# Kernel tuning notes

Measured on AMD Instinct MI355X. Metric: run time of the kernel, lower is better.

## Reference

```python
import jax, jax.numpy as jnp
import numpy as np

N_NODES = 50000


def setup_inputs() -> dict:
    key = jax.random.key(0)
    k1, k2, k3, k4 = jax.random.split(key, 4)
    x = jax.random.normal(k1, (N_NODES, 128), dtype=jnp.float32)
    edge_index = jax.random.randint(k2, (2, 1600000), 0, N_NODES, dtype=jnp.int64)
    W1 = jax.random.normal(k3, (128, 256), dtype=jnp.float32) * (1.0 / np.sqrt(128))
    b1 = jnp.zeros((256,), dtype=jnp.float32)
    W2 = jax.random.normal(k4, (256, 1), dtype=jnp.float32) * (1.0 / np.sqrt(256))
    b2 = jnp.zeros((1,), dtype=jnp.float32)
    return {"x": x, "edge_index": edge_index, "W1": W1, "b1": b1, "W2": W2, "b2": b2}


def _gcn_conv(x, src, dst, norm, W, b, n_nodes):
    # PyG GCNConv: h = X W; out_i = sum_j norm_ij * h_j (+ self loop) + b
    h = x @ W                               # [N, F_out]
    msg = h[src] * norm[:, None]            # [E', F_out] gather + scale
    out = jax.ops.segment_sum(msg, dst, num_segments=n_nodes)  # scatter-add
    return out + b


def reference(x, edge_index, W1, b1, W2, b2):
    n = x.shape[0]
    loop = jnp.arange(n, dtype=edge_index.dtype)
    src = jnp.concatenate([edge_index[0], loop])   # add self loops
    dst = jnp.concatenate([edge_index[1], loop])
    # symmetric degree normalization on A + I
    deg = jax.ops.segment_sum(jnp.ones_like(dst, dtype=x.dtype), dst, num_segments=n)
    dis = jnp.where(deg > 0, jax.lax.rsqrt(deg), 0.0)
    norm = dis[src] * dis[dst]                     # [E']
    h = jax.nn.relu(_gcn_conv(x, src, dst, norm, W1, b1, n))
    return _gcn_conv(h, src, dst, norm, W2, b2, n)
```

## Files before the change

kernel.cpp:

```cpp
#include <hip/hip_runtime.h>


#define EPB_LOG 12
#define EPB (1 << EPB_LOG)
#define BW_LOG 7
#define BW (1 << BW_LOG)
#define MAXBUCK 512
#define SCAN_TILE 2048
#define AMSTRIDE 136

typedef __attribute__((ext_vector_type(8))) short bf16x8;
typedef __attribute__((ext_vector_type(4))) float f32x4;

__device__ inline unsigned short f2bf(float f) {
    unsigned int b = __float_as_uint(f);
    unsigned int r = b + 0x7FFFu + ((b >> 16) & 1u);
    return (unsigned short)(r >> 16);
}
__device__ inline float bf_lo(unsigned int u) { return __uint_as_float(u << 16); }
__device__ inline float bf_hi(unsigned int u) { return __uint_as_float(u & 0xFFFF0000u); }

__device__ inline int detect_stride(const int* edges, int t, int* sh) {
    if (t < 64) {
        int v = edges[2 * t + 1];
        unsigned long long bb = __ballot(v != 0);
        if (t == 0) *sh = bb ? 1 : 2;
    }
    __syncthreads();
    return *sh;
}


__global__ __launch_bounds__(256) void k_count(
        const int* __restrict__ edges, const float* __restrict__ W1,
        unsigned short* __restrict__ w1t, int* __restrict__ btot_raw,
        long long E, int nbuck, int nsb) {
    int b = blockIdx.x, t = threadIdx.x;
    if (b >= nsb) {
        int row = (b - nsb) * 2 + (t >> 7);
        int k = t & 127;
        w1t[row * 128 + k] = f2bf(W1[k * 256 + row]);
        return;
    }
    __shared__ int bins[MAXBUCK];
    __shared__ int sh;
    for (int i = t; i < nbuck; i += 256) bins[i] = 0;
    int stride = detect_stride(edges, t, &sh);
    long long base = (long long)b << EPB_LOG;
    long long rem = E - base;
    int nE = (rem < (long long)EPB) ? (int)rem : EPB;
    for (int i = t; i < nE; i += 256) {
        int d = edges[(E + base + i) * stride];
        atomicAdd(&bins[d >> BW_LOG], 1);
    }
    __syncthreads();
    for (int i = t; i < nbuck; i += 256)
        if (bins[i]) atomicAdd(&btot_raw[i], bins[i]);
}

__global__ __launch_bounds__(256) void k_btot_scan(
        const int* __restrict__ btot_raw, int* __restrict__ btot,
        int* __restrict__ curg, int nbuck) {
    __shared__ int ws4[4];
    int t = threadIdx.x;
    int c4 = (nbuck + 255) >> 8;
    int lo = t * c4;
    int hi = lo + c4; if (hi > nbuck) hi = nbuck;
    if (lo > nbuck) lo = nbuck;
    int vals[2];
    int local = 0;
    for (int i = lo; i < hi; ++i) { vals[i - lo] = btot_raw[i]; local += vals[i - lo]; }
    int lane = t & 63, w = t >> 6;
    int inc = local;
    for (int off = 1; off < 64; off <<= 1) {
        int u = __shfl_up(inc, off, 64);
        if (lane >= off) inc += u;
    }
    if (lane == 63) ws4[w] = inc;
    __syncthreads();
    int woff = 0;
    for (int i = 0; i < w; ++i) woff += ws4[i];
    int ex = woff + inc - local;
    for (int i = lo; i < hi; ++i) {
        btot[i] = ex; curg[i] = ex;
        ex += vals[i - lo];
    }
}

__global__ __launch_bounds__(256) void k_partition(
        const int* __restrict__ edges, int* __restrict__ curg,
        unsigned int* __restrict__ part, long long E, int nbuck) {
    __shared__ unsigned int stage[EPB];
    __shared__ unsigned short dst16[EPB];
    __shared__ int bins[MAXBUCK];
    __shared__ int lcur[MAXBUCK];
    __shared__ int gbase[MAXBUCK];
    __shared__ int ws4[4];
    __shared__ int sh;
    int sb = blockIdx.x, t = threadIdx.x;
    for (int i = t; i < nbuck; i += 256) bins[i] = 0;
    int stride = detect_stride(edges, t, &sh);
    long long base = (long long)sb << EPB_LOG;
    long long rem = E - base;
    int nE = (rem < (long long)EPB) ? (int)rem : EPB;
    for (int i = t; i < nE; i += 256) {
        int d = edges[(E + base + i) * stride];
        dst16[i] = (unsigned short)d;
        atomicAdd(&bins[d >> BW_LOG], 1);
    }
    __syncthreads();
    int c4 = (nbuck + 255) >> 8;
    int lo = t * c4;
    int hi = lo + c4; if (hi > nbuck) hi = nbuck;
    if (lo > nbuck) lo = nbuck;
    int vals[2];
    int local = 0;
    for (int i = lo; i < hi; ++i) { vals[i - lo] = bins[i]; local += vals[i - lo]; }
    for (int i = t; i < nbuck; i += 256) {
        int c = bins[i];
        gbase[i] = c ? atomicAdd(&curg[i], c) : 0;
    }
    __syncthreads();
    int lane = t & 63, w = t >> 6;
    int inc = local;
    for (int off = 1; off < 64; off <<= 1) {
        int u = __shfl_up(inc, off, 64);
        if (lane >= off) inc += u;
    }
    if (lane == 63) ws4[w] = inc;
    __syncthreads();
    int woff = 0;
    for (int i = 0; i < w; ++i) woff += ws4[i];
    int ex = woff + inc - local;
    for (int i = lo; i < hi; ++i) {
        bins[i] = ex;
        lcur[i] = ex;
        ex += vals[i - lo];
    }
    __syncthreads();
    for (int i = t; i < nE; i += 256) {
        int s = edges[(base + i) * stride];
        int d = dst16[i];
        int b = d >> BW_LOG;
        int p = atomicAdd(&lcur[b], 1);
        stage[p] = ((unsigned int)s << 16) | (unsigned int)d;
    }
    __syncthreads();
    for (int i = t; i < nE; i += 256) {
        unsigned int pk = stage[i];
        int b = (int)(pk & 0xFFFFu) >> BW_LOG;
        part[gbase[b] + (i - bins[b])] = pk;
    }
}

__global__ __launch_bounds__(256) void k_build_csr(
        const unsigned int* __restrict__ part, const int* __restrict__ btot,
        const float* __restrict__ x, int* __restrict__ row_start,
        float* __restrict__ dis, int* __restrict__ csr_src,
        unsigned short* __restrict__ xs, int nbuck, int n, long long E) {
    __shared__ int c128[BW];
    __shared__ int lcur[BW];
    __shared__ float dld[BW];
    __shared__ int ws2[2];
    int b = blockIdx.x, t = threadIdx.x;
    if (t < BW) c128[t] = 0;
    __syncthreads();
    int start = btot[b];
    int endp = (b + 1 < nbuck) ? btot[b + 1] : (int)E;
    for (int i = start + t; i < endp; i += 256)
        atomicAdd(&c128[part[i] & (BW - 1)], 1);
    __syncthreads();
    int lane = t & 63, w = t >> 6;
    int deg = (t < BW) ? c128[t] : 0;
    int inc = deg;
    for (int off = 1; off < 64; off <<= 1) {
        int u = __shfl_up(inc, off, 64);
        if (lane >= off) inc += u;
    }
    if (t < BW && lane == 63) ws2[w] = inc;
    __syncthreads();
    if (t < BW) {
        int ex = inc - deg + ((w == 1) ? ws2[0] : 0);
        lcur[t] = ex;
        int d = (b << BW_LOG) + t;
        if (d < n) {
            row_start[d] = start + ex;
            float dv = rsqrtf((float)deg + 1.0f);
            dis[d] = dv;
            dld[t] = dv;
        }
    }
    if (b == nbuck - 1 && t == 0) row_start[n] = (int)E;
    __syncthreads();
    for (int i = start + t; i < endp; i += 256) {
        unsigned int pk = part[i];
        int r = atomicAdd(&lcur[pk & (BW - 1)], 1);
        csr_src[start + r] = (int)(pk >> 16);
    }
    int d0 = b << BW_LOG;
    for (int idx = t; idx < BW * 32; idx += 256) {
        int node = d0 + (idx >> 5);
        if (node >= n) break;
        float dv = dld[idx >> 5];
        float4 v = ((const float4*)x)[(size_t)node * 32 + (idx & 31)];
        ushort4 o;
        o.x = f2bf(v.x * dv); o.y = f2bf(v.y * dv);
        o.z = f2bf(v.z * dv); o.w = f2bf(v.w * dv);
        ((ushort4*)xs)[(size_t)node * 32 + (idx & 31)] = o;
    }
}

__global__ __launch_bounds__(512) void k_agg_mm(
        const unsigned short* __restrict__ xs, const int* __restrict__ csr_src,
        const int* __restrict__ rs, const float* __restrict__ dis,
        const unsigned short* __restrict__ w1t, const float* __restrict__ b1,
        const float* __restrict__ W2, float* __restrict__ svs, int n) {
    __shared__ short am[64 * AMSTRIDE];
    int t = threadIdx.x;
    int lane = t & 63, w = t >> 6;
    int blk = blockIdx.x;
    const unsigned int* xsu = (const unsigned int*)xs;
#pragma unroll 1
    for (int jj = 0; jj < 8; ++jj) {
        int r = w * 8 + jj;
        int node = blk * 64 + r;
        unsigned int pack = 0;
        if (node < n) {
            int start = rs[node], end = rs[node + 1];
            unsigned int self = xsu[((size_t)node << 6) + lane];
            float a0 = bf_lo(self), a1 = bf_hi(self);
            int e = start;
            for (; e + 7 < end; e += 8) {
                int s0 = csr_src[e],     s1 = csr_src[e + 1];
                int s2 = csr_src[e + 2], s3 = csr_src[e + 3];
                int s4 = csr_src[e + 4], s5 = csr_src[e + 5];
                int s6 = csr_src[e + 6], s7 = csr_src[e + 7];
                unsigned int v0 = xsu[((size_t)s0 << 6) + lane];
                unsigned int v1 = xsu[((size_t)s1 << 6) + lane];
                unsigned int v2 = xsu[((size_t)s2 << 6) + lane];
                unsigned int v3 = xsu[((size_t)s3 << 6) + lane];
                unsigned int v4 = xsu[((size_t)s4 << 6) + lane];
                unsigned int v5 = xsu[((size_t)s5 << 6) + lane];
                unsigned int v6 = xsu[((size_t)s6 << 6) + lane];
                unsigned int v7 = xsu[((size_t)s7 << 6) + lane];
                a0 += bf_lo(v0); a1 += bf_hi(v0);
                a0 += bf_lo(v1); a1 += bf_hi(v1);
                a0 += bf_lo(v2); a1 += bf_hi(v2);
                a0 += bf_lo(v3); a1 += bf_hi(v3);
                a0 += bf_lo(v4); a1 += bf_hi(v4);
                a0 += bf_lo(v5); a1 += bf_hi(v5);
                a0 += bf_lo(v6); a1 += bf_hi(v6);
                a0 += bf_lo(v7); a1 += bf_hi(v7);
            }
            for (; e < end; ++e) {
                int s0 = csr_src[e];
                unsigned int v0 = xsu[((size_t)s0 << 6) + lane];
                a0 += bf_lo(v0); a1 += bf_hi(v0);
            }
            float dn = dis[node];
            pack = (unsigned int)f2bf(a0 * dn) | ((unsigned int)f2bf(a1 * dn) << 16);
        }
        *(unsigned int*)&am[r * AMSTRIDE + 2 * lane] = pack;
    }
    __syncthreads();
    if (w >= 4) return;
    int m = lane & 15;
    int quad = lane >> 4;
    int node0 = blk * 64 + w * 16;

    bf16x8 afrag[4];
    const short* arow = &am[(w * 16 + m) * AMSTRIDE + quad * 8];
#pragma unroll
    for (int ks = 0; ks < 4; ++ks)
        afrag[ks] = *(const bf16x8*)(arow + ks * 32);

    float p0 = 0.f, p1 = 0.f, p2 = 0.f, p3 = 0.f;
#pragma unroll 1
    for (int tt = 0; tt < 16; ++tt) {
        const unsigned short* brow = w1t + (size_t)(tt * 16 + m) * 128 + quad * 8;
        f32x4 acc = {0.f, 0.f, 0.f, 0.f};
#pragma unroll
        for (int ks = 0; ks < 4; ++ks) {
            bf16x8 bfrag = *(const bf16x8*)(brow + ks * 32);
            acc = __builtin_amdgcn_mfma_f32_16x16x32_bf16(afrag[ks], bfrag, acc, 0, 0, 0);
        }
        int col = tt * 16 + m;
        float bb = b1[col], w2 = W2[col];
        float h0 = acc[0] + bb, h1 = acc[1] + bb, h2 = acc[2] + bb, h3 = acc[3] + bb;
        p0 += (h0 > 0.f ? h0 : 0.f) * w2;
        p1 += (h1 > 0.f ? h1 : 0.f) * w2;
        p2 += (h2 > 0.f ? h2 : 0.f) * w2;
        p3 += (h3 > 0.f ? h3 : 0.f) * w2;
    }
#pragma unroll
    for (int off = 1; off < 16; off <<= 1) {
        p0 += __shfl_xor(p0, off, 64);
        p1 += __shfl_xor(p1, off, 64);
        p2 += __shfl_xor(p2, off, 64);
        p3 += __shfl_xor(p3, off, 64);
    }
    if (m == 0) {
        int nb = node0 + quad * 4;
        if (nb + 0 < n) svs[nb + 0] = p0 * dis[nb + 0];
        if (nb + 1 < n) svs[nb + 1] = p1 * dis[nb + 1];
        if (nb + 2 < n) svs[nb + 2] = p2 * dis[nb + 2];
        if (nb + 3 < n) svs[nb + 3] = p3 * dis[nb + 3];
    }
}

__global__ __launch_bounds__(256) void k_out(
        const float* __restrict__ svs, const int* __restrict__ csr_src,
        const int* __restrict__ row_start, const float* __restrict__ dis,
        const float* __restrict__ b2, float* __restrict__ out, int n) {
    int wid  = (blockIdx.x * blockDim.x + threadIdx.x) >> 6;
    int lane = threadIdx.x & 63;
    if (wid >= n) return;
    int start = row_start[wid], end = row_start[wid + 1];
    float acc = 0.f;
    for (int e = start + lane; e < end; e += 64)
        acc += svs[csr_src[e]];
    for (int off = 32; off; off >>= 1) acc += __shfl_down(acc, off, 64);
    if (lane == 0)
        out[wid] = dis[wid] * (acc + svs[wid]) + b2[0];
}

__global__ void k_init(const int* __restrict__ edges, int* __restrict__ flag,
                       int* __restrict__ cnt, int n) {
    int i = blockIdx.x * blockDim.x + threadIdx.x;
    if (i < n) cnt[i] = 0;
    if (blockIdx.x == 0 && threadIdx.x < 64) {
        int v = edges[2 * threadIdx.x + 1];
        unsigned long long b = __ballot(v != 0);
        if (threadIdx.x == 0) flag[0] = b ? 1 : 2;
    }
}
__global__ __launch_bounds__(128) void k_prep_w(const float* __restrict__ W1,
        unsigned short* __restrict__ w1t) {
    int nn = blockIdx.x, k = threadIdx.x;
    w1t[nn * 128 + k] = f2bf(W1[k * 256 + nn]);
}
__global__ __launch_bounds__(256) void k_prep_xs(const float* __restrict__ x,
        const float* __restrict__ dis, unsigned short* __restrict__ xs, int n) {
    int i = blockIdx.x * 256 + threadIdx.x;
    if (i >= n * 32) return;
    float dsc = dis[i >> 5];
    float4 v = ((const float4*)x)[i];
    ushort4 o;
    o.x = f2bf(v.x * dsc); o.y = f2bf(v.y * dsc);
    o.z = f2bf(v.z * dsc); o.w = f2bf(v.w * dsc);
    ((ushort4*)xs)[i] = o;
}
__global__ void k_count_slow(const int* __restrict__ edges, const int* __restrict__ flag,
                             int* __restrict__ cnt, int* __restrict__ posi, long long E) {
    long long e = (long long)blockIdx.x * blockDim.x + threadIdx.x;
    if (e >= E) return;
    int stride = flag[0];
    int d = edges[(E + e) * stride];
    posi[e] = atomicAdd(&cnt[d], 1);
}
__global__ __launch_bounds__(256) void k_scan_partial(
        const int* __restrict__ cnt, int* __restrict__ bsum, int n) {
    int t = threadIdx.x;
    int idx = blockIdx.x * SCAN_TILE + t * 8;
    int s = 0;
#pragma unroll
    for (int j = 0; j < 8; ++j) { int i = idx + j; if (i < n) s += cnt[i]; }
    for (int off = 32; off; off >>= 1) s += __shfl_down(s, off, 64);
    __shared__ int ws[4];
    if ((t & 63) == 0) ws[t >> 6] = s;
    __syncthreads();
    if (t == 0) bsum[blockIdx.x] = ws[0] + ws[1] + ws[2] + ws[3];
}
__global__ void k_scan_tops(int* __restrict__ bsum, int nb) {
    int t = threadIdx.x;
    int w = (t < nb) ? bsum[t] : 0;
    int v = w;
    for (int off = 1; off < 64; off <<= 1) {
        int u = __shfl_up(v, off, 64);
        if (t >= off) v += u;
    }
    if (t < nb) bsum[t] = v - w;
}
__global__ __launch_bounds__(256) void k_scan_apply(
        const int* __restrict__ cnt, const int* __restrict__ bsum,
        int* __restrict__ row_start, float* __restrict__ dis, int n) {
    int t = threadIdx.x;
    int lane = t & 63, w = t >> 6;
    int idx = blockIdx.x * SCAN_TILE + t * 8;
    int vals[8];
    int s = 0;
#pragma unroll
    for (int j = 0; j < 8; ++j) { int i = idx + j; vals[j] = (i < n) ? cnt[i] : 0; s += vals[j]; }
    int inc = s;
    for (int off = 1; off < 64; off <<= 1) {
        int u = __shfl_up(inc, off, 64);
        if (lane >= off) inc += u;
    }
    __shared__ int wsum[4];
    if (lane == 63) wsum[w] = inc;
    __syncthreads();
    int woff = 0;
    for (int i = 0; i < w; ++i) woff += wsum[i];
    int ex = bsum[blockIdx.x] + woff + inc - s;
#pragma unroll
    for (int j = 0; j < 8; ++j) {
        int i = idx + j;
        if (i < n) {
            row_start[i] = ex;
            dis[i] = rsqrtf((float)vals[j] + 1.0f);
            ex += vals[j];
        }
    }
    if (idx <= n && n < idx + 8) row_start[n] = ex;
}
__global__ void k_scatter_slow(const int* __restrict__ edges, const int* __restrict__ flag,
                               const int* __restrict__ row_start, const int* __restrict__ posi,
                               int* __restrict__ csr_src, long long E) {
    long long e = (long long)blockIdx.x * blockDim.x + threadIdx.x;
    if (e >= E) return;
    int stride = flag[0];
    int s = edges[e * stride];
    int d = edges[(E + e) * stride];
    csr_src[row_start[d] + posi[e]] = s;
}
__global__ __launch_bounds__(256) void k_agg(
        const unsigned short* __restrict__ xs, const int* __restrict__ csr_src,
        const int* __restrict__ row_start, const float* __restrict__ dis,
        unsigned short* __restrict__ aggh, int n) {
    int wid  = (blockIdx.x * blockDim.x + threadIdx.x) >> 6;
    int lane = threadIdx.x & 63;
    if (wid >= n) return;
    int start = row_start[wid], end = row_start[wid + 1];
    unsigned int self = ((const unsigned int*)xs)[((size_t)wid << 6) + lane];
    float a0 = bf_lo(self), a1 = bf_hi(self);
    for (int e = start; e < end; ++e) {
        int s0 = csr_src[e];
        unsigned int v0 = ((const unsigned int*)xs)[((size_t)s0 << 6) + lane];
        a0 += bf_lo(v0); a1 += bf_hi(v0);
    }
    float dn = dis[wid];
    unsigned int pack = (unsigned int)f2bf(a0 * dn) | ((unsigned int)f2bf(a1 * dn) << 16);
    ((unsigned int*)aggh)[((size_t)wid << 6) + lane] = pack;
}
__global__ __launch_bounds__(256) void k_mm(
        const unsigned short* __restrict__ aggh, const unsigned short* __restrict__ w1t,
        const float* __restrict__ b1, const float* __restrict__ W2,
        const float* __restrict__ dis, float* __restrict__ svs, int n) {
    int wave = threadIdx.x >> 6;
    int lane = threadIdx.x & 63;
    int m = lane & 15, quad = lane >> 4;
    int node0 = blockIdx.x * 64 + wave * 16;
    bf16x8 afrag[4];
    const unsigned short* arow = aggh + (size_t)(node0 + m) * 128 + quad * 8;
#pragma unroll
    for (int ks = 0; ks < 4; ++ks) afrag[ks] = *(const bf16x8*)(arow + ks * 32);
    float p0 = 0.f, p1 = 0.f, p2 = 0.f, p3 = 0.f;
#pragma unroll 1
    for (int tt = 0; tt < 16; ++tt) {
        const unsigned short* brow = w1t + (size_t)(tt * 16 + m) * 128 + quad * 8;
        f32x4 acc = {0.f, 0.f, 0.f, 0.f};
#pragma unroll
        for (int ks = 0; ks < 4; ++ks) {
            bf16x8 bfrag = *(const bf16x8*)(brow + ks * 32);
            acc = __builtin_amdgcn_mfma_f32_16x16x32_bf16(afrag[ks], bfrag, acc, 0, 0, 0);
        }
        int col = tt * 16 + m;
        float bb = b1[col], w2 = W2[col];
        float h0 = acc[0] + bb, h1 = acc[1] + bb, h2 = acc[2] + bb, h3 = acc[3] + bb;
        p0 += (h0 > 0.f ? h0 : 0.f) * w2;
        p1 += (h1 > 0.f ? h1 : 0.f) * w2;
        p2 += (h2 > 0.f ? h2 : 0.f) * w2;
        p3 += (h3 > 0.f ? h3 : 0.f) * w2;
    }
#pragma unroll
    for (int off = 1; off < 16; off <<= 1) {
        p0 += __shfl_xor(p0, off, 64);
        p1 += __shfl_xor(p1, off, 64);
        p2 += __shfl_xor(p2, off, 64);
        p3 += __shfl_xor(p3, off, 64);
    }
    if (m == 0) {
        int nb = node0 + quad * 4;
        if (nb + 0 < n) svs[nb + 0] = p0 * dis[nb + 0];
        if (nb + 1 < n) svs[nb + 1] = p1 * dis[nb + 1];
        if (nb + 2 < n) svs[nb + 2] = p2 * dis[nb + 2];
        if (nb + 3 < n) svs[nb + 3] = p3 * dis[nb + 3];
    }
}

extern "C" void kernel_launch(void* const* d_in, const int* in_sizes, int n_in,
                              void* d_out, int out_size, void* d_ws, size_t ws_size,
                              hipStream_t stream) {
    const float* x  = (const float*)d_in[0];
    const int*   ei = (const int*)d_in[1];
    const float* W1 = (const float*)d_in[2];
    const float* b1 = (const float*)d_in[3];
    const float* W2 = (const float*)d_in[4];
    const float* b2 = (const float*)d_in[5];
    float* out = (float*)d_out;

    const int N = in_sizes[0] / 128;
    const long long E = in_sizes[1] / 2;
    const int nsb = (int)((E + EPB - 1) >> EPB_LOG);
    const int nbuck = (N + BW - 1) >> BW_LOG;

    char* ws = (char*)d_ws;
    size_t off = 0;
    auto take = [&](size_t bytes) -> char* {
        char* p = ws + off;
        off = (off + bytes + 255) & ~(size_t)255;
        return p;
    };
    int*            flag     = (int*)take(4);
    int*            cnt      = (int*)take((size_t)N * 4);
    int*            rs       = (int*)take((size_t)(N + 1) * 4);
    float*          dis      = (float*)take((size_t)N * 4);
    float*          svs      = (float*)take((size_t)N * 4);
    int*            bsum     = (int*)take(64 * 4);
    int*            btot_raw = (int*)take(MAXBUCK * 4);
    int*            btot     = (int*)take(MAXBUCK * 4);
    int*            curg     = (int*)take(MAXBUCK * 4);
    unsigned int*   part     = (unsigned int*)take((size_t)E * 4);
    int*            csr_src  = (int*)take((size_t)E * 4);
    unsigned short* xs       = (unsigned short*)take((size_t)N * 128 * 2);
    unsigned short* w1t      = (unsigned short*)take((size_t)256 * 128 * 2);
    unsigned short* aggh     = (unsigned short*)take((size_t)(N + 64) * 128 * 2);

    int nb_n  = (N + 255) / 256;
    int nb_e  = (int)((E + 255) / 256);
    int nb_s  = (N + SCAN_TILE - 1) / SCAN_TILE;
    int nb_x  = (N * 32 + 255) / 256;
    int nb_am = (N + 63) / 64;

    bool fast = (N < 65536);

    if (fast) {
        hipMemsetAsync(btot_raw, 0, (size_t)nbuck * 4, stream);
        k_count    <<<nsb + 128, 256, 0, stream>>>(ei, W1, w1t, btot_raw, E, nbuck, nsb);
        k_btot_scan<<<1, 256, 0, stream>>>(btot_raw, btot, curg, nbuck);
        k_partition<<<nsb, 256, 0, stream>>>(ei, curg, part, E, nbuck);
        k_build_csr<<<nbuck, 256, 0, stream>>>(part, btot, x, rs, dis, csr_src,
                                               xs, nbuck, N, E);
        k_agg_mm   <<<nb_am, 512, 0, stream>>>(xs, csr_src, rs, dis, w1t, b1, W2, svs, N);
        k_out      <<<(N + 3) / 4, 256, 0, stream>>>(svs, csr_src, rs, dis, b2, out, N);
    } else {
        k_init        <<<nb_n, 256, 0, stream>>>(ei, flag, cnt, N);
        k_prep_w      <<<256, 128, 0, stream>>>(W1, w1t);
        k_count_slow  <<<nb_e, 256, 0, stream>>>(ei, flag, cnt, (int*)part, E);
        k_scan_partial<<<nb_s, 256, 0, stream>>>(cnt, bsum, N);
        k_scan_tops   <<<1, 64, 0, stream>>>(bsum, nb_s);
        k_scan_apply  <<<nb_s, 256, 0, stream>>>(cnt, bsum, rs, dis, N);
        k_prep_xs     <<<nb_x, 256, 0, stream>>>(x, dis, xs, N);
        k_scatter_slow<<<nb_e, 256, 0, stream>>>(ei, flag, rs, (const int*)part, csr_src, E);
        k_agg         <<<(N + 3) / 4, 256, 0, stream>>>(xs, csr_src, rs, dis, aggh, N);
        k_mm          <<<(N + 63) / 64, 256, 0, stream>>>(aggh, w1t, b1, W2, dis, svs, N);
        k_out         <<<(N + 3) / 4, 256, 0, stream>>>(svs, csr_src, rs, dis, b2, out, N);
    }
}
```

Before: 237.8 us.

## Split fused aggregation-matmul kernel into separate aggregation and MFMA kernels

Replaces the fused k_agg_mm kernel, which staged 64 aggregated rows in LDS before running MFMA on four of its eight waves, with two kernels. The first is a one-wave-per-node aggregation kernel (keeping the 8-way unrolled gather) that writes bf16 results to a global buffer. The second is the existing MFMA kernel, which reads that buffer. This removes the block-wide barrier and the idle half of the block during the matmul phase, and lets the gather kernel run at finer granularity, at the cost of an extra global round trip of N×128 bf16 and one more launch.

```diff
diff --git a/kernel.cpp b/kernel.cpp
--- a/kernel.cpp
+++ b/kernel.cpp
@@ -7,7 +7,6 @@
 #define BW (1 << BW_LOG)
 #define MAXBUCK 512
 #define SCAN_TILE 2048
-#define AMSTRIDE 136
 
 typedef __attribute__((ext_vector_type(8))) short bf16x8;
 typedef __attribute__((ext_vector_type(4))) float f32x4;
@@ -210,66 +209,63 @@
     }
 }
 
-__global__ __launch_bounds__(512) void k_agg_mm(
+__global__ __launch_bounds__(256) void k_agg(
         const unsigned short* __restrict__ xs, const int* __restrict__ csr_src,
-        const int* __restrict__ rs, const float* __restrict__ dis,
-        const unsigned short* __restrict__ w1t, const float* __restrict__ b1,
-        const float* __restrict__ W2, float* __restrict__ svs, int n) {
-    __shared__ short am[64 * AMSTRIDE];
-    int t = threadIdx.x;
-    int lane = t & 63, w = t >> 6;
-    int blk = blockIdx.x;
+        const int* __restrict__ row_start, const float* __restrict__ dis,
+        unsigned short* __restrict__ aggh, int n) {
+    int wid  = (blockIdx.x * blockDim.x + threadIdx.x) >> 6;
+    int lane = threadIdx.x & 63;
+    if (wid >= n) return;
+    int start = row_start[wid], end = row_start[wid + 1];
     const unsigned int* xsu = (const unsigned int*)xs;
-#pragma unroll 1
-    for (int jj = 0; jj < 8; ++jj) {
-        int r = w * 8 + jj;
-        int node = blk * 64 + r;
-        unsigned int pack = 0;
-        if (node < n) {
-            int start = rs[node], end = rs[node + 1];
-            unsigned int self = xsu[((size_t)node << 6) + lane];
-            float a0 = bf_lo(self), a1 = bf_hi(self);
-            int e = start;
-            for (; e + 7 < end; e += 8) {
-                int s0 = csr_src[e],     s1 = csr_src[e + 1];
-                int s2 = csr_src[e + 2], s3 = csr_src[e + 3];
-                int s4 = csr_src[e + 4], s5 = csr_src[e + 5];
-                int s6 = csr_src[e + 6], s7 = csr_src[e + 7];
-                unsigned int v0 = xsu[((size_t)s0 << 6) + lane];
-                unsigned int v1 = xsu[((size_t)s1 << 6) + lane];
-                unsigned int v2 = xsu[((size_t)s2 << 6) + lane];
-                unsigned int v3 = xsu[((size_t)s3 << 6) + lane];
-                unsigned int v4 = xsu[((size_t)s4 << 6) + lane];
-                unsigned int v5 = xsu[((size_t)s5 << 6) + lane];
-                unsigned int v6 = xsu[((size_t)s6 << 6) + lane];
-                unsigned int v7 = xsu[((size_t)s7 << 6) + lane];
-                a0 += bf_lo(v0); a1 += bf_hi(v0);
-                a0 += bf_lo(v1); a1 += bf_hi(v1);
-                a0 += bf_lo(v2); a1 += bf_hi(v2);
-                a0 += bf_lo(v3); a1 += bf_hi(v3);
-                a0 += bf_lo(v4); a1 += bf_hi(v4);
-                a0 += bf_lo(v5); a1 += bf_hi(v5);
-                a0 += bf_lo(v6); a1 += bf_hi(v6);
-                a0 += bf_lo(v7); a1 += bf_hi(v7);
-            }
-            for (; e < end; ++e) {
-                int s0 = csr_src[e];
-                unsigned int v0 = xsu[((size_t)s0 << 6) + lane];
-                a0 += bf_lo(v0); a1 += bf_hi(v0);
-            }
-            float dn = dis[node];
-            pack = (unsigned int)f2bf(a0 * dn) | ((unsigned int)f2bf(a1 * dn) << 16);
-        }
-        *(unsigned int*)&am[r * AMSTRIDE + 2 * lane] = pack;
-    }
-    __syncthreads();
-    if (w >= 4) return;
-    int m = lane & 15;
+    unsigned int self = xsu[((size_t)wid << 6) + lane];
+    float acc0 = bf_lo(self);
+    float acc1 = bf_hi(self);
+    int e = start;
+    for (; e + 7 < end; e += 8) {
+        int s0 = csr_src[e],     s1 = csr_src[e + 1];
+        int s2 = csr_src[e + 2], s3 = csr_src[e + 3];
+        int s4 = csr_src[e + 4], s5 = csr_src[e + 5];
+        int s6 = csr_src[e + 6], s7 = csr_src[e + 7];
+        unsigned int v0 = xsu[((size_t)s0 << 6) + lane];
+        unsigned int v1 = xsu[((size_t)s1 << 6) + lane];
+        unsigned int v2 = xsu[((size_t)s2 << 6) + lane];
+        unsigned int v3 = xsu[((size_t)s3 << 6) + lane];
+        unsigned int v4 = xsu[((size_t)s4 << 6) + lane];
+        unsigned int v5 = xsu[((size_t)s5 << 6) + lane];
+        unsigned int v6 = xsu[((size_t)s6 << 6) + lane];
+        unsigned int v7 = xsu[((size_t)s7 << 6) + lane];
+        acc0 += bf_lo(v0); acc1 += bf_hi(v0);
+        acc0 += bf_lo(v1); acc1 += bf_hi(v1);
+        acc0 += bf_lo(v2); acc1 += bf_hi(v2);
+        acc0 += bf_lo(v3); acc1 += bf_hi(v3);
+        acc0 += bf_lo(v4); acc1 += bf_hi(v4);
+        acc0 += bf_lo(v5); acc1 += bf_hi(v5);
+        acc0 += bf_lo(v6); acc1 += bf_hi(v6);
+        acc0 += bf_lo(v7); acc1 += bf_hi(v7);
+    }
+    for (; e < end; ++e) {
+        int s0 = csr_src[e];
+        unsigned int v0 = xsu[((size_t)s0 << 6) + lane];
+        acc0 += bf_lo(v0); acc1 += bf_hi(v0);
+    }
+    float dn = dis[wid];
+    unsigned int pack = (unsigned int)f2bf(acc0 * dn) | ((unsigned int)f2bf(acc1 * dn) << 16);
+    ((unsigned int*)aggh)[((size_t)wid << 6) + lane] = pack;
+}
+
+__global__ __launch_bounds__(256) void k_mm(
+        const unsigned short* __restrict__ aggh, const unsigned short* __restrict__ w1t,
+        const float* __restrict__ b1, const float* __restrict__ W2,
+        const float* __restrict__ dis, float* __restrict__ svs, int n) {
+    int wave = threadIdx.x >> 6;
+    int lane = threadIdx.x & 63;
+    int m    = lane & 15;
     int quad = lane >> 4;
-    int node0 = blk * 64 + w * 16;
+    int node0 = blockIdx.x * 64 + wave * 16;
 
     bf16x8 afrag[4];
-    const short* arow = &am[(w * 16 + m) * AMSTRIDE + quad * 8];
+    const unsigned short* arow = aggh + (size_t)(node0 + m) * 128 + quad * 8;
 #pragma unroll
     for (int ks = 0; ks < 4; ++ks)
         afrag[ks] = *(const bf16x8*)(arow + ks * 32);
@@ -422,70 +418,6 @@
     int s = edges[e * stride];
     int d = edges[(E + e) * stride];
     csr_src[row_start[d] + posi[e]] = s;
-}
-__global__ __launch_bounds__(256) void k_agg(
-        const unsigned short* __restrict__ xs, const int* __restrict__ csr_src,
-        const int* __restrict__ row_start, const float* __restrict__ dis,
-        unsigned short* __restrict__ aggh, int n) {
-    int wid  = (blockIdx.x * blockDim.x + threadIdx.x) >> 6;
-    int lane = threadIdx.x & 63;
-    if (wid >= n) return;
-    int start = row_start[wid], end = row_start[wid + 1];
-    unsigned int self = ((const unsigned int*)xs)[((size_t)wid << 6) + lane];
-    float a0 = bf_lo(self), a1 = bf_hi(self);
-    for (int e = start; e < end; ++e) {
-        int s0 = csr_src[e];
-        unsigned int v0 = ((const unsigned int*)xs)[((size_t)s0 << 6) + lane];
-        a0 += bf_lo(v0); a1 += bf_hi(v0);
-    }
-    float dn = dis[wid];
-    unsigned int pack = (unsigned int)f2bf(a0 * dn) | ((unsigned int)f2bf(a1 * dn) << 16);
-    ((unsigned int*)aggh)[((size_t)wid << 6) + lane] = pack;
-}
-__global__ __launch_bounds__(256) void k_mm(
-        const unsigned short* __restrict__ aggh, const unsigned short* __restrict__ w1t,
-        const float* __restrict__ b1, const float* __restrict__ W2,
-        const float* __restrict__ dis, float* __restrict__ svs, int n) {
-    int wave = threadIdx.x >> 6;
-    int lane = threadIdx.x & 63;
-    int m = lane & 15, quad = lane >> 4;
-    int node0 = blockIdx.x * 64 + wave * 16;
-    bf16x8 afrag[4];
-    const unsigned short* arow = aggh + (size_t)(node0 + m) * 128 + quad * 8;
-#pragma unroll
-    for (int ks = 0; ks < 4; ++ks) afrag[ks] = *(const bf16x8*)(arow + ks * 32);
-    float p0 = 0.f, p1 = 0.f, p2 = 0.f, p3 = 0.f;
-#pragma unroll 1
-    for (int tt = 0; tt < 16; ++tt) {
-        const unsigned short* brow = w1t + (size_t)(tt * 16 + m) * 128 + quad * 8;
-        f32x4 acc = {0.f, 0.f, 0.f, 0.f};
-#pragma unroll
-        for (int ks = 0; ks < 4; ++ks) {
-            bf16x8 bfrag = *(const bf16x8*)(brow + ks * 32);
-            acc = __builtin_amdgcn_mfma_f32_16x16x32_bf16(afrag[ks], bfrag, acc, 0, 0, 0);
-        }
-        int col = tt * 16 + m;
-        float bb = b1[col], w2 = W2[col];
-        float h0 = acc[0] + bb, h1 = acc[1] + bb, h2 = acc[2] + bb, h3 = acc[3] + bb;
-        p0 += (h0 > 0.f ? h0 : 0.f) * w2;
-        p1 += (h1 > 0.f ? h1 : 0.f) * w2;
-        p2 += (h2 > 0.f ? h2 : 0.f) * w2;
-        p3 += (h3 > 0.f ? h3 : 0.f) * w2;
-    }
-#pragma unroll
-    for (int off = 1; off < 16; off <<= 1) {
-        p0 += __shfl_xor(p0, off, 64);
-        p1 += __shfl_xor(p1, off, 64);
-        p2 += __shfl_xor(p2, off, 64);
-        p3 += __shfl_xor(p3, off, 64);
-    }
-    if (m == 0) {
-        int nb = node0 + quad * 4;
-        if (nb + 0 < n) svs[nb + 0] = p0 * dis[nb + 0];
-        if (nb + 1 < n) svs[nb + 1] = p1 * dis[nb + 1];
-        if (nb + 2 < n) svs[nb + 2] = p2 * dis[nb + 2];
-        if (nb + 3 < n) svs[nb + 3] = p3 * dis[nb + 3];
-    }
 }
 
 extern "C" void kernel_launch(void* const* d_in, const int* in_sizes, int n_in,
@@ -530,7 +462,7 @@
     int nb_e  = (int)((E + 255) / 256);
     int nb_s  = (N + SCAN_TILE - 1) / SCAN_TILE;
     int nb_x  = (N * 32 + 255) / 256;
-    int nb_am = (N + 63) / 64;
+    int nb_mm = (N + 63) / 64;
 
     bool fast = (N < 65536);
 
@@ -541,7 +473,8 @@
         k_partition<<<nsb, 256, 0, stream>>>(ei, curg, part, E, nbuck);
         k_build_csr<<<nbuck, 256, 0, stream>>>(part, btot, x, rs, dis, csr_src,
                                                xs, nbuck, N, E);
-        k_agg_mm   <<<nb_am, 512, 0, stream>>>(xs, csr_src, rs, dis, w1t, b1, W2, svs, N);
+        k_agg      <<<(N + 3) / 4, 256, 0, stream>>>(xs, csr_src, rs, dis, aggh, N);
+        k_mm       <<<nb_mm, 256, 0, stream>>>(aggh, w1t, b1, W2, dis, svs, N);
         k_out      <<<(N + 3) / 4, 256, 0, stream>>>(svs, csr_src, rs, dis, b2, out, N);
     } else {
         k_init        <<<nb_n, 256, 0, stream>>>(ei, flag, cnt, N);
@@ -553,7 +486,7 @@
         k_prep_xs     <<<nb_x, 256, 0, stream>>>(x, dis, xs, N);
         k_scatter_slow<<<nb_e, 256, 0, stream>>>(ei, flag, rs, (const int*)part, csr_src, E);
         k_agg         <<<(N + 3) / 4, 256, 0, stream>>>(xs, csr_src, rs, dis, aggh, N);
-        k_mm          <<<(N + 63) / 64, 256, 0, stream>>>(aggh, w1t, b1, W2, dis, svs, N);
+        k_mm          <<<nb_mm, 256, 0, stream>>>(aggh, w1t, b1, W2, dis, svs, N);
         k_out         <<<(N + 3) / 4, 256, 0, stream>>>(svs, csr_src, rs, dis, b2, out, N);
     }
 }
```

New measurement: 242.0 us. Within noise of the previous version (+1.7%).

## Shrink agg_mm blocks to 16 nodes and split MFMA columns across all waves

Applied to the files above, without the earlier changes.

Restructures the fused aggregate+matmul kernel so each 256-thread block handles 16 nodes instead of 64. All four waves now take part in the MFMA stage, each computing 64 of the 256 hidden columns, with partial W2 dot products combined through shared memory. Previously half the waves idled during the matmul and every active wave looped over all 16 column tiles. The change trades that idle time for an extra barrier and redundant W1 fragment loads per block, plus about four times as many blocks.

```diff
diff --git a/kernel.cpp b/kernel.cpp
--- a/kernel.cpp
+++ b/kernel.cpp
@@ -7,7 +7,7 @@
 #define BW (1 << BW_LOG)
 #define MAXBUCK 512
 #define SCAN_TILE 2048
-#define AMSTRIDE 136
+#define AMS 136
 
 typedef __attribute__((ext_vector_type(8))) short bf16x8;
 typedef __attribute__((ext_vector_type(4))) float f32x4;
@@ -210,20 +210,21 @@
     }
 }
 
-__global__ __launch_bounds__(512) void k_agg_mm(
+__global__ __launch_bounds__(256) void k_agg_mm(
         const unsigned short* __restrict__ xs, const int* __restrict__ csr_src,
         const int* __restrict__ rs, const float* __restrict__ dis,
         const unsigned short* __restrict__ w1t, const float* __restrict__ b1,
         const float* __restrict__ W2, float* __restrict__ svs, int n) {
-    __shared__ short am[64 * AMSTRIDE];
+    __shared__ short am[16 * AMS];
+    __shared__ float psum[4][16];
     int t = threadIdx.x;
     int lane = t & 63, w = t >> 6;
-    int blk = blockIdx.x;
+    int node0 = blockIdx.x * 16;
     const unsigned int* xsu = (const unsigned int*)xs;
 #pragma unroll 1
-    for (int jj = 0; jj < 8; ++jj) {
-        int r = w * 8 + jj;
-        int node = blk * 64 + r;
+    for (int j = 0; j < 4; ++j) {
+        int r = w * 4 + j;
+        int node = node0 + r;
         unsigned int pack = 0;
         if (node < n) {
             int start = rs[node], end = rs[node + 1];
@@ -260,52 +261,50 @@
             float dn = dis[node];
             pack = (unsigned int)f2bf(a0 * dn) | ((unsigned int)f2bf(a1 * dn) << 16);
         }
-        *(unsigned int*)&am[r * AMSTRIDE + 2 * lane] = pack;
-    }
-    __syncthreads();
-    if (w >= 4) return;
+        *(unsigned int*)&am[r * AMS + 2 * lane] = pack;
+    }
+    __syncthreads();
     int m = lane & 15;
     int quad = lane >> 4;
-    int node0 = blk * 64 + w * 16;
-
     bf16x8 afrag[4];
-    const short* arow = &am[(w * 16 + m) * AMSTRIDE + quad * 8];
 #pragma unroll
     for (int ks = 0; ks < 4; ++ks)
-        afrag[ks] = *(const bf16x8*)(arow + ks * 32);
-
-    float p0 = 0.f, p1 = 0.f, p2 = 0.f, p3 = 0.f;
-#pragma unroll 1
-    for (int tt = 0; tt < 16; ++tt) {
-        const unsigned short* brow = w1t + (size_t)(tt * 16 + m) * 128 + quad * 8;
+        afrag[ks] = *(const bf16x8*)&am[m * AMS + quad * 8 + ks * 32];
+    float pacc0 = 0.f, pacc1 = 0.f, pacc2 = 0.f, pacc3 = 0.f;
+#pragma unroll
+    for (int tt = 0; tt < 4; ++tt) {
+        int col = w * 64 + tt * 16 + m;
+        const unsigned short* brow = w1t + (size_t)col * 128 + quad * 8;
         f32x4 acc = {0.f, 0.f, 0.f, 0.f};
 #pragma unroll
         for (int ks = 0; ks < 4; ++ks) {
             bf16x8 bfrag = *(const bf16x8*)(brow + ks * 32);
             acc = __builtin_amdgcn_mfma_f32_16x16x32_bf16(afrag[ks], bfrag, acc, 0, 0, 0);
         }
-        int col = tt * 16 + m;
         float bb = b1[col], w2 = W2[col];
         float h0 = acc[0] + bb, h1 = acc[1] + bb, h2 = acc[2] + bb, h3 = acc[3] + bb;
-        p0 += (h0 > 0.f ? h0 : 0.f) * w2;
-        p1 += (h1 > 0.f ? h1 : 0.f) * w2;
-        p2 += (h2 > 0.f ? h2 : 0.f) * w2;
-        p3 += (h3 > 0.f ? h3 : 0.f) * w2;
+        pacc0 += (h0 > 0.f ? h0 : 0.f) * w2;
+        pacc1 += (h1 > 0.f ? h1 : 0.f) * w2;
+        pacc2 += (h2 > 0.f ? h2 : 0.f) * w2;
+        pacc3 += (h3 > 0.f ? h3 : 0.f) * w2;
     }
 #pragma unroll
     for (int off = 1; off < 16; off <<= 1) {
-        p0 += __shfl_xor(p0, off, 64);
-        p1 += __shfl_xor(p1, off, 64);
-        p2 += __shfl_xor(p2, off, 64);
-        p3 += __shfl_xor(p3, off, 64);
+        pacc0 += __shfl_xor(pacc0, off, 64);
+        pacc1 += __shfl_xor(pacc1, off, 64);
+        pacc2 += __shfl_xor(pacc2, off, 64);
+        pacc3 += __shfl_xor(pacc3, off, 64);
     }
     if (m == 0) {
-        int nb = node0 + quad * 4;
-        if (nb + 0 < n) svs[nb + 0] = p0 * dis[nb + 0];
-        if (nb + 1 < n) svs[nb + 1] = p1 * dis[nb + 1];
-        if (nb + 2 < n) svs[nb + 2] = p2 * dis[nb + 2];
-        if (nb + 3 < n) svs[nb + 3] = p3 * dis[nb + 3];
-    }
+        psum[w][quad * 4 + 0] = pacc0;
+        psum[w][quad * 4 + 1] = pacc1;
+        psum[w][quad * 4 + 2] = pacc2;
+        psum[w][quad * 4 + 3] = pacc3;
+    }
+    __syncthreads();
+    if (t < 16 && node0 + t < n)
+        svs[node0 + t] = (psum[0][t] + psum[1][t] + psum[2][t] + psum[3][t])
+                         * dis[node0 + t];
 }
 
 __global__ __launch_bounds__(256) void k_out(
@@ -431,11 +430,12 @@
     int lane = threadIdx.x & 63;
     if (wid >= n) return;
     int start = row_start[wid], end = row_start[wid + 1];
-    unsigned int self = ((const unsigned int*)xs)[((size_t)wid << 6) + lane];
+    const unsigned int* xsu = (const unsigned int*)xs;
+    unsigned int self = xsu[((size_t)wid << 6) + lane];
     float a0 = bf_lo(self), a1 = bf_hi(self);
     for (int e = start; e < end; ++e) {
         int s0 = csr_src[e];
-        unsigned int v0 = ((const unsigned int*)xs)[((size_t)s0 << 6) + lane];
+        unsigned int v0 = xsu[((size_t)s0 << 6) + lane];
         a0 += bf_lo(v0); a1 += bf_hi(v0);
     }
     float dn = dis[wid];
@@ -530,7 +530,6 @@
     int nb_e  = (int)((E + 255) / 256);
     int nb_s  = (N + SCAN_TILE - 1) / SCAN_TILE;
     int nb_x  = (N * 32 + 255) / 256;
-    int nb_am = (N + 63) / 64;
 
     bool fast = (N < 65536);
 
@@ -541,7 +540,8 @@
         k_partition<<<nsb, 256, 0, stream>>>(ei, curg, part, E, nbuck);
         k_build_csr<<<nbuck, 256, 0, stream>>>(part, btot, x, rs, dis, csr_src,
                                                xs, nbuck, N, E);
-        k_agg_mm   <<<nb_am, 512, 0, stream>>>(xs, csr_src, rs, dis, w1t, b1, W2, svs, N);
+        k_agg_mm   <<<(N + 15) / 16, 256, 0, stream>>>(xs, csr_src, rs, dis,
+                                                       w1t, b1, W2, svs, N);
         k_out      <<<(N + 3) / 4, 256, 0, stream>>>(svs, csr_src, rs, dis, b2, out, N);
     } else {
         k_init        <<<nb_n, 256, 0, stream>>>(ei, flag, cnt, N);
```

After: 248.6 us. 1.05x slower.
